# Optimization experiments

Measured on AMD Instinct MI355X. Metric: run time of the kernel, lower is better.

## Reference

```python
import jax, jax.numpy as jnp
import numpy as np

NUM_HEADS = 16


def setup_inputs() -> dict:
    key = jax.random.key(0)
    ks = jax.random.split(key, 5)
    B, S, D = 2, 2048, 2048
    scale = 1.0 / np.sqrt(D)
    return {
        "x": jax.random.normal(ks[0], (B, S, D), dtype=jnp.float32),
        "W_q": jax.random.normal(ks[1], (D, D), dtype=jnp.float32) * scale,
        "W_k": jax.random.normal(ks[2], (D, D), dtype=jnp.float32) * scale,
        "W_v": jax.random.normal(ks[3], (D, D), dtype=jnp.float32) * scale,
        "W_o": jax.random.normal(ks[4], (D, D), dtype=jnp.float32) * scale,
        "b_o": jnp.zeros((D,), dtype=jnp.float32),
    }


def reference(x, W_q, W_k, W_v, W_o, b_o):
    B, S, D = x.shape
    H = NUM_HEADS
    hd = D // H
    # projections, split into heads: [B, H, S, hd]
    q = (x @ W_q).reshape(B, S, H, hd).transpose(0, 2, 1, 3)
    k = (x @ W_k).reshape(B, S, H, hd).transpose(0, 2, 1, 3)
    v = (x @ W_v).reshape(B, S, H, hd).transpose(0, 2, 1, 3)
    # causal attention with explicit score matrix [B, H, S, S]
    scores = jnp.einsum("bhqd,bhkd->bhqk", q, k) / jnp.sqrt(jnp.asarray(hd, x.dtype))
    causal = jnp.tril(jnp.ones((S, S), dtype=bool))  # True = keep
    scores = jnp.where(causal, scores, -jnp.inf)
    weights = jax.nn.softmax(scores, axis=-1)
    ctx = jnp.einsum("bhqk,bhkd->bhqd", weights, v)
    ctx = ctx.transpose(0, 2, 1, 3).reshape(B, S, D)
    return ctx @ W_o + b_o
```

## Files before the change

kernel.cpp:

```cpp
#include <hip/hip_runtime.h>
#include <stdint.h>

#define SQ_S 2048
#define DIM 2048
#define NH 16
#define HD 128
#define NB 2
#define NROWS (NB * SQ_S)
#define NQKV (3 * DIM)

typedef __bf16 bf16x8 __attribute__((ext_vector_type(8)));
typedef float f32x4 __attribute__((ext_vector_type(4)));
typedef unsigned short u16;

__device__ __forceinline__ u16 f2bf(float f) {
    unsigned int u = __float_as_uint(f);
    u += 0x7FFF + ((u >> 16) & 1);
    return (u16)(u >> 16);
}

__device__ __forceinline__ void load_lds16(const u16* g, u16* lds) {
    __builtin_amdgcn_global_load_lds(
        (const __attribute__((address_space(1))) unsigned int*)(uintptr_t)g,
        (__attribute__((address_space(3))) unsigned int*)(unsigned int)(uintptr_t)lds,
        16, 0, 0);
}

__global__ __launch_bounds__(256) void cast_x_kernel(const float* __restrict__ in,
                                                     u16* __restrict__ out) {
    int i = (blockIdx.x * 256 + threadIdx.x) * 4;
    float4 v = *(const float4*)(in + i);
    ushort4 o;
    o.x = f2bf(v.x); o.y = f2bf(v.y); o.z = f2bf(v.z); o.w = f2bf(v.w);
    *(ushort4*)(out + i) = o;
}

__global__ __launch_bounds__(256) void transpose_w_kernel(
    const float* __restrict__ w0, const float* __restrict__ w1,
    const float* __restrict__ w2, const float* __restrict__ w3,
    u16* __restrict__ o0, u16* __restrict__ o1,
    u16* __restrict__ o2, u16* __restrict__ o3) {
    __shared__ u16 tile[64][65];
    int z = blockIdx.z;
    const float* in = z == 0 ? w0 : z == 1 ? w1 : z == 2 ? w2 : w3;
    u16* out = z == 0 ? o0 : z == 1 ? o1 : z == 2 ? o2 : o3;
    int r0 = blockIdx.y * 64, c0 = blockIdx.x * 64;
    int t = threadIdx.x;
#pragma unroll
    for (int i = 0; i < 16; ++i) {
        int idx = i * 256 + t;
        int r = idx >> 6, c = idx & 63;
        tile[r][c] = f2bf(in[(size_t)(r0 + r) * DIM + c0 + c]);
    }
    __syncthreads();
#pragma unroll
    for (int i = 0; i < 4; ++i) {
        int idx = i * 256 + t;
        int oc = idx >> 4;
        int r4 = (idx & 15) * 4;
        ushort4 v;
        v.x = tile[r4 + 0][oc]; v.y = tile[r4 + 1][oc];
        v.z = tile[r4 + 2][oc]; v.w = tile[r4 + 3][oc];
        *(ushort4*)(out + (size_t)(c0 + oc) * DIM + r0 + r4) = v;
    }
}

__global__ __launch_bounds__(256) void transpose_v_kernel(const u16* __restrict__ V,
                                                          u16* __restrict__ Vt, int ldv) {
    __shared__ u16 tile[64][72];
    int s0 = blockIdx.x * 64, d0 = blockIdx.y * 64;
    int bh = blockIdx.z;
    int b = bh >> 4, h = bh & 15;
    int t = threadIdx.x;
#pragma unroll
    for (int i = 0; i < 16; ++i) {
        int idx = i * 256 + t;
        int r = idx >> 6, c = idx & 63;
        tile[r][c] = V[((size_t)(b * SQ_S + s0 + r)) * ldv + h * HD + d0 + c];
    }
    __syncthreads();
#pragma unroll
    for (int i = 0; i < 16; ++i) {
        int idx = i * 256 + t;
        int r = idx >> 6, c = idx & 63;
        Vt[((size_t)(bh * HD + d0 + r)) * SQ_S + s0 + c] = tile[c][r];
    }
}

__global__ __launch_bounds__(256) void gemm_bt_bf16(const u16* __restrict__ A,
                                                    const u16* __restrict__ Bt,
                                                    u16* __restrict__ C,
                                                    int M, int N, int K) {
    __shared__ u16 As[128 * 64];
    __shared__ u16 Bs[128 * 64];
    int t = threadIdx.x;
    int w = t >> 6, l = t & 63;
    int wm = (w >> 1) * 64, wn = (w & 1) * 64;
    int lr = l & 15, q = l >> 4;
    int bm = blockIdx.y, bn = blockIdx.x;
    int st_gcol = (((t & 7) ^ ((t >> 3) & 7)) * 8);
    f32x4 acc[4][4] = {};

    for (int k0 = 0; k0 < K; k0 += 64) {
        __syncthreads();
#pragma unroll
        for (int c = 0; c < 4; ++c) {
            int e = c * 2048 + t * 8;
            int row = e >> 6;
            load_lds16(A + (size_t)(bm * 128 + row) * K + k0 + st_gcol, As + e);
        }
#pragma unroll
        for (int c = 0; c < 4; ++c) {
            int e = c * 2048 + t * 8;
            int row = e >> 6;
            load_lds16(Bt + (size_t)(bn * 128 + row) * K + k0 + st_gcol, Bs + e);
        }
        __syncthreads();
#pragma unroll
        for (int kk = 0; kk < 2; ++kk) {
            bf16x8 a[4], b[4];
#pragma unroll
            for (int mt = 0; mt < 4; ++mt)
                a[mt] = *(const bf16x8*)(As + (wm + mt * 16 + lr) * 64 +
                                         (((kk * 4 + q) ^ (lr & 7)) * 8));
#pragma unroll
            for (int nt = 0; nt < 4; ++nt)
                b[nt] = *(const bf16x8*)(Bs + (wn + nt * 16 + lr) * 64 +
                                         (((kk * 4 + q) ^ (lr & 7)) * 8));
#pragma unroll
            for (int mt = 0; mt < 4; ++mt)
#pragma unroll
                for (int nt = 0; nt < 4; ++nt)
                    acc[mt][nt] = __builtin_amdgcn_mfma_f32_16x16x32_bf16(a[mt], b[nt], acc[mt][nt], 0, 0, 0);
        }
    }
    int r0 = bm * 128 + wm, c0 = bn * 128 + wn;
#pragma unroll
    for (int mt = 0; mt < 4; ++mt)
#pragma unroll
        for (int nt = 0; nt < 4; ++nt)
#pragma unroll
            for (int r = 0; r < 4; ++r) {
                int row = r0 + mt * 16 + q * 4 + r;
                int col = c0 + nt * 16 + lr;
                C[(size_t)row * N + col] = f2bf(acc[mt][nt][r]);
            }
}

__global__ __launch_bounds__(256) void gemm_bt_f32b(const u16* __restrict__ A,
                                                    const u16* __restrict__ Bt,
                                                    float* __restrict__ C,
                                                    const float* __restrict__ bias,
                                                    int M, int N, int K) {
    __shared__ u16 As[128 * 64];
    __shared__ u16 Bs[128 * 64];
    int t = threadIdx.x;
    int w = t >> 6, l = t & 63;
    int wm = (w >> 1) * 64, wn = (w & 1) * 64;
    int lr = l & 15, q = l >> 4;
    int bm = blockIdx.y, bn = blockIdx.x;
    int st_gcol = (((t & 7) ^ ((t >> 3) & 7)) * 8);
    f32x4 acc[4][4] = {};

    for (int k0 = 0; k0 < K; k0 += 64) {
        __syncthreads();
#pragma unroll
        for (int c = 0; c < 4; ++c) {
            int e = c * 2048 + t * 8;
            int row = e >> 6;
            load_lds16(A + (size_t)(bm * 128 + row) * K + k0 + st_gcol, As + e);
        }
#pragma unroll
        for (int c = 0; c < 4; ++c) {
            int e = c * 2048 + t * 8;
            int row = e >> 6;
            load_lds16(Bt + (size_t)(bn * 128 + row) * K + k0 + st_gcol, Bs + e);
        }
        __syncthreads();
#pragma unroll
        for (int kk = 0; kk < 2; ++kk) {
            bf16x8 a[4], b[4];
#pragma unroll
            for (int mt = 0; mt < 4; ++mt)
                a[mt] = *(const bf16x8*)(As + (wm + mt * 16 + lr) * 64 +
                                         (((kk * 4 + q) ^ (lr & 7)) * 8));
#pragma unroll
            for (int nt = 0; nt < 4; ++nt)
                b[nt] = *(const bf16x8*)(Bs + (wn + nt * 16 + lr) * 64 +
                                         (((kk * 4 + q) ^ (lr & 7)) * 8));
#pragma unroll
            for (int mt = 0; mt < 4; ++mt)
#pragma unroll
                for (int nt = 0; nt < 4; ++nt)
                    acc[mt][nt] = __builtin_amdgcn_mfma_f32_16x16x32_bf16(a[mt], b[nt], acc[mt][nt], 0, 0, 0);
        }
    }
    int r0 = bm * 128 + wm, c0 = bn * 128 + wn;
#pragma unroll
    for (int mt = 0; mt < 4; ++mt)
#pragma unroll
        for (int nt = 0; nt < 4; ++nt)
#pragma unroll
            for (int r = 0; r < 4; ++r) {
                int row = r0 + mt * 16 + q * 4 + r;
                int col = c0 + nt * 16 + lr;
                C[(size_t)row * N + col] = acc[mt][nt][r] + bias[col];
            }
}

__global__ __launch_bounds__(256) void attn_kernel(const u16* __restrict__ Q,
                                                   const u16* __restrict__ K,
                                                   const u16* __restrict__ Vt,
                                                   u16* __restrict__ ctx, int ldqk) {
    __shared__ u16 Kl[2][64 * 128];
    __shared__ u16 Vl[2][128 * 64];
    __shared__ u16 Pl[4][16 * 64];
    int t = threadIdx.x;
    int w = t >> 6, l = t & 63;
    int lr = l & 15, q = l >> 4, lk = q * 8;
    int bid = blockIdx.x;
    int r_  = bid >> 3;
    int px  = r_ & 15;
    int h   = (bid & 7) + ((r_ >> 4) & 1) * 8;
    int b   = r_ >> 5;
    const float scale = 0.08838834764831845f;
    int stK_gcol = (((t & 15) ^ (t >> 4)) * 8);
    int stV_gcol = (((t & 7) ^ ((t >> 3) & 7)) * 8);
    const u16* Kbase = K + (size_t)b * SQ_S * ldqk + h * HD;
    const u16* Vbase = Vt + ((size_t)(b * NH + h)) * HD * SQ_S;

#pragma unroll 1
    for (int pass = 0; pass < 2; ++pass) {
        int qt = pass == 0 ? px : 31 - px;
        int q0 = qt * 64;
        int njt = qt + 1;

        bf16x8 qf[4];
        {
            const u16* qp = Q + ((size_t)(b * SQ_S + q0 + w * 16 + lr)) * ldqk + h * HD;
#pragma unroll
            for (int kd = 0; kd < 4; ++kd)
                qf[kd] = *(const bf16x8*)(qp + kd * 32 + lk);
        }

        f32x4 o[8] = {};
        float l_r[4] = {0.f, 0.f, 0.f, 0.f};

        {
            int e = t * 8;
#pragma unroll
            for (int c = 0; c < 4; ++c) {
                int eK = c * 2048 + e;
                load_lds16(Kbase + (size_t)(eK >> 7) * ldqk + stK_gcol, Kl[0] + eK);
            }
#pragma unroll
            for (int c = 0; c < 4; ++c) {
                int eV = c * 2048 + e;
                load_lds16(Vbase + (size_t)(eV >> 6) * SQ_S + stV_gcol, Vl[0] + eV);
            }
        }

#pragma unroll 1
        for (int jt = 0; jt < njt; ++jt) {
            __syncthreads();
            if (jt + 1 < njt) {
                int j1 = (jt + 1) * 64;
                u16* Kd = Kl[(jt + 1) & 1];
                u16* Vd = Vl[(jt + 1) & 1];
                int e = t * 8;
#pragma unroll
                for (int c = 0; c < 4; ++c) {
                    int eK = c * 2048 + e;
                    load_lds16(Kbase + (size_t)(j1 + (eK >> 7)) * ldqk + stK_gcol, Kd + eK);
                }
#pragma unroll
                for (int c = 0; c < 4; ++c) {
                    int eV = c * 2048 + e;
                    load_lds16(Vbase + (size_t)(eV >> 6) * SQ_S + j1 + stV_gcol, Vd + eV);
                }
            }
            const u16* Kc = Kl[jt & 1];
            const u16* Vc = Vl[jt & 1];

            f32x4 s[4] = {};
#pragma unroll
            for (int kd = 0; kd < 4; ++kd) {
#pragma unroll
                for (int nt = 0; nt < 4; ++nt) {
                    bf16x8 kb = *(const bf16x8*)(Kc + (nt * 16 + lr) * 128 +
                                                 (((kd * 4 + q) ^ lr) * 8));
                    s[nt] = __builtin_amdgcn_mfma_f32_16x16x32_bf16(qf[kd], kb, s[nt], 0, 0, 0);
                }
            }
            bool diag = (jt == qt);
            float rs[4] = {0.f, 0.f, 0.f, 0.f};
            float pv[4][4];
#pragma unroll
            for (int nt = 0; nt < 4; ++nt)
#pragma unroll
                for (int r = 0; r < 4; ++r) {
                    float v = s[nt][r] * scale - 6.0f;
                    if (diag && (nt * 16 + lr > w * 16 + q * 4 + r)) v = -1.0e30f;
                    float pp = __expf(v);
                    pv[nt][r] = pp;
                    rs[r] += pp;
                }
#pragma unroll
            for (int d = 1; d < 16; d <<= 1)
#pragma unroll
                for (int r = 0; r < 4; ++r)
                    rs[r] += __shfl_xor(rs[r], d, 64);
#pragma unroll
            for (int r = 0; r < 4; ++r)
                l_r[r] += rs[r];
            u16* pw = Pl[w];
#pragma unroll
            for (int nt = 0; nt < 4; ++nt)
#pragma unroll
                for (int r = 0; r < 4; ++r) {
                    int prow = q * 4 + r;
                    int pcol = nt * 16 + lr;
                    pw[prow * 64 + (((pcol >> 3) ^ (prow & 7)) * 8) + (pcol & 7)] = f2bf(pv[nt][r]);
                }
            asm volatile("s_waitcnt lgkmcnt(0)" ::: "memory");
#pragma unroll
            for (int kj = 0; kj < 2; ++kj) {
                bf16x8 pa = *(const bf16x8*)(pw + lr * 64 + (((kj * 4 + q) ^ (lr & 7)) * 8));
#pragma unroll
                for (int nd = 0; nd < 8; ++nd) {
                    bf16x8 vb = *(const bf16x8*)(Vc + (nd * 16 + lr) * 64 +
                                                 (((kj * 4 + q) ^ (lr & 7)) * 8));
                    o[nd] = __builtin_amdgcn_mfma_f32_16x16x32_bf16(pa, vb, o[nd], 0, 0, 0);
                }
            }
        }
        float li[4];
#pragma unroll
        for (int r = 0; r < 4; ++r) li[r] = 1.f / l_r[r];
#pragma unroll
        for (int nd = 0; nd < 8; ++nd)
#pragma unroll
            for (int r = 0; r < 4; ++r) {
                int row = q0 + w * 16 + q * 4 + r;
                int col = h * HD + nd * 16 + lr;
                ctx[((size_t)(b * SQ_S + row)) * DIM + col] = f2bf(o[nd][r] * li[r]);
            }
        __syncthreads();
    }
}

extern "C" void kernel_launch(void* const* d_in, const int* in_sizes, int n_in,
                              void* d_out, int out_size, void* d_ws, size_t ws_size,
                              hipStream_t stream) {
    const float* x  = (const float*)d_in[0];
    const float* Wq = (const float*)d_in[1];
    const float* Wk = (const float*)d_in[2];
    const float* Wv = (const float*)d_in[3];
    const float* Wo = (const float*)d_in[4];
    const float* bo = (const float*)d_in[5];
    float* out = (float*)d_out;

    char* p = (char*)d_ws;
    const size_t SZ_ACT  = (size_t)NROWS * DIM * 2;
    const size_t SZ_W    = (size_t)DIM * DIM * 2;
    const size_t SZ_QKV  = (size_t)NROWS * NQKV * 2;
    u16* Xb   = (u16*)(p);
    u16* Wqkv = (u16*)(p + SZ_ACT);
    u16* Wot  = (u16*)(p + SZ_ACT + 3 * SZ_W);
    u16* QKV  = (u16*)(p + SZ_ACT + 4 * SZ_W);
    u16* Vt   = (u16*)(p + SZ_ACT + 4 * SZ_W + SZ_QKV);
    u16* Cx   = (u16*)(p + 2 * SZ_ACT + 4 * SZ_W + SZ_QKV);

    cast_x_kernel<<<(NROWS * DIM) / 1024, 256, 0, stream>>>(x, Xb);
    transpose_w_kernel<<<dim3(DIM / 64, DIM / 64, 4), 256, 0, stream>>>(
        Wq, Wk, Wv, Wo,
        Wqkv, Wqkv + (size_t)DIM * DIM, Wqkv + 2 * (size_t)DIM * DIM, Wot);
    gemm_bt_bf16<<<dim3(NQKV / 128, NROWS / 128), 256, 0, stream>>>(Xb, Wqkv, QKV, NROWS, NQKV, DIM);
    transpose_v_kernel<<<dim3(SQ_S / 64, HD / 64, NB * NH), 256, 0, stream>>>(QKV + 2 * DIM, Vt, NQKV);
    attn_kernel<<<512, 256, 0, stream>>>(QKV, QKV + DIM, Vt, Cx, NQKV);
    gemm_bt_f32b<<<dim3(DIM / 128, NROWS / 128), 256, 0, stream>>>(Cx, Wot, out, bo, NROWS, DIM, DIM);
}
```

Before: 382.2 us.

## Fuse V transpose into QKV GEMM epilogue and switch GEMMs to 32x32 MFMA

The QKV projection GEMM now writes Q and K into a compact buffer and writes V directly in transposed per-head layout from its epilogue, which removes the separate transpose_v kernel and its extra read and write of V. Both GEMMs also move from 16x16x32 to 32x32x16 bf16 MFMA tiles, halving the LDS fragment loads per MFMA. The transposed V stores are 8-byte ushort4 writes strided by sequence length, so they may coalesce less well than the row-major stores they replace.

```diff
diff --git a/kernel.cpp b/kernel.cpp
--- a/kernel.cpp
+++ b/kernel.cpp
@@ -8,9 +8,11 @@
 #define NB 2
 #define NROWS (NB * SQ_S)
 #define NQKV (3 * DIM)
+#define NQK (2 * DIM)
 
 typedef __bf16 bf16x8 __attribute__((ext_vector_type(8)));
 typedef float f32x4 __attribute__((ext_vector_type(4)));
+typedef float f32x16 __attribute__((ext_vector_type(16)));
 typedef unsigned short u16;
 
 __device__ __forceinline__ u16 f2bf(float f) {
@@ -65,41 +67,20 @@
     }
 }
 
-__global__ __launch_bounds__(256) void transpose_v_kernel(const u16* __restrict__ V,
-                                                          u16* __restrict__ Vt, int ldv) {
-    __shared__ u16 tile[64][72];
-    int s0 = blockIdx.x * 64, d0 = blockIdx.y * 64;
-    int bh = blockIdx.z;
-    int b = bh >> 4, h = bh & 15;
-    int t = threadIdx.x;
-#pragma unroll
-    for (int i = 0; i < 16; ++i) {
-        int idx = i * 256 + t;
-        int r = idx >> 6, c = idx & 63;
-        tile[r][c] = V[((size_t)(b * SQ_S + s0 + r)) * ldv + h * HD + d0 + c];
-    }
-    __syncthreads();
-#pragma unroll
-    for (int i = 0; i < 16; ++i) {
-        int idx = i * 256 + t;
-        int r = idx >> 6, c = idx & 63;
-        Vt[((size_t)(bh * HD + d0 + r)) * SQ_S + s0 + c] = tile[c][r];
-    }
-}
-
-__global__ __launch_bounds__(256) void gemm_bt_bf16(const u16* __restrict__ A,
-                                                    const u16* __restrict__ Bt,
-                                                    u16* __restrict__ C,
-                                                    int M, int N, int K) {
+__global__ __launch_bounds__(256) void gemm_qkv(const u16* __restrict__ A,
+                                                const u16* __restrict__ Bt,
+                                                u16* __restrict__ QKo,
+                                                u16* __restrict__ Vt) {
     __shared__ u16 As[128 * 64];
     __shared__ u16 Bs[128 * 64];
+    const int K = DIM;
     int t = threadIdx.x;
     int w = t >> 6, l = t & 63;
     int wm = (w >> 1) * 64, wn = (w & 1) * 64;
-    int lr = l & 15, q = l >> 4;
+    int m32 = l & 31, kh = l >> 5;
     int bm = blockIdx.y, bn = blockIdx.x;
     int st_gcol = (((t & 7) ^ ((t >> 3) & 7)) * 8);
-    f32x4 acc[4][4] = {};
+    f32x16 acc[2][2] = {};
 
     for (int k0 = 0; k0 < K; k0 += 64) {
         __syncthreads();
@@ -117,50 +98,72 @@
         }
         __syncthreads();
 #pragma unroll
-        for (int kk = 0; kk < 2; ++kk) {
-            bf16x8 a[4], b[4];
-#pragma unroll
-            for (int mt = 0; mt < 4; ++mt)
-                a[mt] = *(const bf16x8*)(As + (wm + mt * 16 + lr) * 64 +
-                                         (((kk * 4 + q) ^ (lr & 7)) * 8));
-#pragma unroll
-            for (int nt = 0; nt < 4; ++nt)
-                b[nt] = *(const bf16x8*)(Bs + (wn + nt * 16 + lr) * 64 +
-                                         (((kk * 4 + q) ^ (lr & 7)) * 8));
-#pragma unroll
-            for (int mt = 0; mt < 4; ++mt)
-#pragma unroll
-                for (int nt = 0; nt < 4; ++nt)
-                    acc[mt][nt] = __builtin_amdgcn_mfma_f32_16x16x32_bf16(a[mt], b[nt], acc[mt][nt], 0, 0, 0);
+        for (int ks = 0; ks < 4; ++ks) {
+            bf16x8 a[2], b[2];
+#pragma unroll
+            for (int mt = 0; mt < 2; ++mt)
+                a[mt] = *(const bf16x8*)(As + (wm + mt * 32 + m32) * 64 +
+                                         (((ks * 2 + kh) ^ (m32 & 7)) * 8));
+#pragma unroll
+            for (int nt = 0; nt < 2; ++nt)
+                b[nt] = *(const bf16x8*)(Bs + (wn + nt * 32 + m32) * 64 +
+                                         (((ks * 2 + kh) ^ (m32 & 7)) * 8));
+#pragma unroll
+            for (int mt = 0; mt < 2; ++mt)
+#pragma unroll
+                for (int nt = 0; nt < 2; ++nt)
+                    acc[mt][nt] = __builtin_amdgcn_mfma_f32_32x32x16_bf16(a[mt], b[nt], acc[mt][nt], 0, 0, 0);
         }
     }
     int r0 = bm * 128 + wm, c0 = bn * 128 + wn;
-#pragma unroll
-    for (int mt = 0; mt < 4; ++mt)
-#pragma unroll
-        for (int nt = 0; nt < 4; ++nt)
-#pragma unroll
-            for (int r = 0; r < 4; ++r) {
-                int row = r0 + mt * 16 + q * 4 + r;
-                int col = c0 + nt * 16 + lr;
-                C[(size_t)row * N + col] = f2bf(acc[mt][nt][r]);
-            }
-}
-
-__global__ __launch_bounds__(256) void gemm_bt_f32b(const u16* __restrict__ A,
-                                                    const u16* __restrict__ Bt,
-                                                    float* __restrict__ C,
-                                                    const float* __restrict__ bias,
-                                                    int M, int N, int K) {
+    if (bn < 32) {
+#pragma unroll
+        for (int mt = 0; mt < 2; ++mt)
+#pragma unroll
+            for (int nt = 0; nt < 2; ++nt) {
+                int col = c0 + nt * 32 + m32;
+#pragma unroll
+                for (int i = 0; i < 16; ++i) {
+                    int row = r0 + mt * 32 + (i & 3) + 8 * (i >> 2) + 4 * kh;
+                    QKo[(size_t)row * NQK + col] = f2bf(acc[mt][nt][i]);
+                }
+            }
+    } else {
+#pragma unroll
+        for (int mt = 0; mt < 2; ++mt)
+#pragma unroll
+            for (int nt = 0; nt < 2; ++nt) {
+                int colv = c0 + nt * 32 + m32 - 4096;
+                int h = colv >> 7, dd = colv & 127;
+#pragma unroll
+                for (int g = 0; g < 4; ++g) {
+                    int row = r0 + mt * 32 + 8 * g + 4 * kh;
+                    int b = row >> 11, s = row & 2047;
+                    ushort4 v4;
+                    v4.x = f2bf(acc[mt][nt][g * 4 + 0]);
+                    v4.y = f2bf(acc[mt][nt][g * 4 + 1]);
+                    v4.z = f2bf(acc[mt][nt][g * 4 + 2]);
+                    v4.w = f2bf(acc[mt][nt][g * 4 + 3]);
+                    *(ushort4*)(Vt + (((size_t)(b * NH + h) * HD + dd) * SQ_S + s)) = v4;
+                }
+            }
+    }
+}
+
+__global__ __launch_bounds__(256) void gemm_out(const u16* __restrict__ A,
+                                                const u16* __restrict__ Bt,
+                                                float* __restrict__ C,
+                                                const float* __restrict__ bias) {
     __shared__ u16 As[128 * 64];
     __shared__ u16 Bs[128 * 64];
+    const int K = DIM, N = DIM;
     int t = threadIdx.x;
     int w = t >> 6, l = t & 63;
     int wm = (w >> 1) * 64, wn = (w & 1) * 64;
-    int lr = l & 15, q = l >> 4;
+    int m32 = l & 31, kh = l >> 5;
     int bm = blockIdx.y, bn = blockIdx.x;
     int st_gcol = (((t & 7) ^ ((t >> 3) & 7)) * 8);
-    f32x4 acc[4][4] = {};
+    f32x16 acc[2][2] = {};
 
     for (int k0 = 0; k0 < K; k0 += 64) {
         __syncthreads();
@@ -178,34 +181,36 @@
         }
         __syncthreads();
 #pragma unroll
-        for (int kk = 0; kk < 2; ++kk) {
-            bf16x8 a[4], b[4];
-#pragma unroll
-            for (int mt = 0; mt < 4; ++mt)
-                a[mt] = *(const bf16x8*)(As + (wm + mt * 16 + lr) * 64 +
-                                         (((kk * 4 + q) ^ (lr & 7)) * 8));
-#pragma unroll
-            for (int nt = 0; nt < 4; ++nt)
-                b[nt] = *(const bf16x8*)(Bs + (wn + nt * 16 + lr) * 64 +
-                                         (((kk * 4 + q) ^ (lr & 7)) * 8));
-#pragma unroll
-            for (int mt = 0; mt < 4; ++mt)
-#pragma unroll
-                for (int nt = 0; nt < 4; ++nt)
-                    acc[mt][nt] = __builtin_amdgcn_mfma_f32_16x16x32_bf16(a[mt], b[nt], acc[mt][nt], 0, 0, 0);
+        for (int ks = 0; ks < 4; ++ks) {
+            bf16x8 a[2], b[2];
+#pragma unroll
+            for (int mt = 0; mt < 2; ++mt)
+                a[mt] = *(const bf16x8*)(As + (wm + mt * 32 + m32) * 64 +
+                                         (((ks * 2 + kh) ^ (m32 & 7)) * 8));
+#pragma unroll
+            for (int nt = 0; nt < 2; ++nt)
+                b[nt] = *(const bf16x8*)(Bs + (wn + nt * 32 + m32) * 64 +
+                                         (((ks * 2 + kh) ^ (m32 & 7)) * 8));
+#pragma unroll
+            for (int mt = 0; mt < 2; ++mt)
+#pragma unroll
+                for (int nt = 0; nt < 2; ++nt)
+                    acc[mt][nt] = __builtin_amdgcn_mfma_f32_32x32x16_bf16(a[mt], b[nt], acc[mt][nt], 0, 0, 0);
         }
     }
     int r0 = bm * 128 + wm, c0 = bn * 128 + wn;
 #pragma unroll
-    for (int mt = 0; mt < 4; ++mt)
-#pragma unroll
-        for (int nt = 0; nt < 4; ++nt)
-#pragma unroll
-            for (int r = 0; r < 4; ++r) {
-                int row = r0 + mt * 16 + q * 4 + r;
-                int col = c0 + nt * 16 + lr;
-                C[(size_t)row * N + col] = acc[mt][nt][r] + bias[col];
-            }
+    for (int mt = 0; mt < 2; ++mt)
+#pragma unroll
+        for (int nt = 0; nt < 2; ++nt) {
+            int col = c0 + nt * 32 + m32;
+            float bb = bias[col];
+#pragma unroll
+            for (int i = 0; i < 16; ++i) {
+                int row = r0 + mt * 32 + (i & 3) + 8 * (i >> 2) + 4 * kh;
+                C[(size_t)row * N + col] = acc[mt][nt][i] + bb;
+            }
+        }
 }
 
 __global__ __launch_bounds__(256) void attn_kernel(const u16* __restrict__ Q,
@@ -361,22 +366,20 @@
     float* out = (float*)d_out;
 
     char* p = (char*)d_ws;
-    const size_t SZ_ACT  = (size_t)NROWS * DIM * 2;
-    const size_t SZ_W    = (size_t)DIM * DIM * 2;
-    const size_t SZ_QKV  = (size_t)NROWS * NQKV * 2;
+    const size_t SZ_ACT = (size_t)NROWS * DIM * 2;
+    const size_t SZ_W   = (size_t)DIM * DIM * 2;
     u16* Xb   = (u16*)(p);
     u16* Wqkv = (u16*)(p + SZ_ACT);
     u16* Wot  = (u16*)(p + SZ_ACT + 3 * SZ_W);
-    u16* QKV  = (u16*)(p + SZ_ACT + 4 * SZ_W);
-    u16* Vt   = (u16*)(p + SZ_ACT + 4 * SZ_W + SZ_QKV);
-    u16* Cx   = (u16*)(p + 2 * SZ_ACT + 4 * SZ_W + SZ_QKV);
+    u16* QK   = (u16*)(p + SZ_ACT + 4 * SZ_W);
+    u16* Vt   = (u16*)(p + 3 * SZ_ACT + 4 * SZ_W);
+    u16* Cx   = (u16*)(p + 4 * SZ_ACT + 4 * SZ_W);
 
     cast_x_kernel<<<(NROWS * DIM) / 1024, 256, 0, stream>>>(x, Xb);
     transpose_w_kernel<<<dim3(DIM / 64, DIM / 64, 4), 256, 0, stream>>>(
         Wq, Wk, Wv, Wo,
         Wqkv, Wqkv + (size_t)DIM * DIM, Wqkv + 2 * (size_t)DIM * DIM, Wot);
-    gemm_bt_bf16<<<dim3(NQKV / 128, NROWS / 128), 256, 0, stream>>>(Xb, Wqkv, QKV, NROWS, NQKV, DIM);
-    transpose_v_kernel<<<dim3(SQ_S / 64, HD / 64, NB * NH), 256, 0, stream>>>(QKV + 2 * DIM, Vt, NQKV);
-    attn_kernel<<<512, 256, 0, stream>>>(QKV, QKV + DIM, Vt, Cx, NQKV);
-    gemm_bt_f32b<<<dim3(DIM / 128, NROWS / 128), 256, 0, stream>>>(Cx, Wot, out, bo, NROWS, DIM, DIM);
-}
+    gemm_qkv<<<dim3(NQKV / 128, NROWS / 128), 256, 0, stream>>>(Xb, Wqkv, QK, Vt);
+    attn_kernel<<<512, 256, 0, stream>>>(QK, QK + DIM, Vt, Cx, NQK);
+    gemm_out<<<dim3(DIM / 128, NROWS / 128), 256, 0, stream>>>(Cx, Wot, out, bo);
+}
```

Measured after the change: 373.2 us. 1.02x faster.
